# Kernel tuning notes

Hardware: AMD Instinct MI355X
Metric: run time of the kernel (lower is better)

## Reference

```python
import jax, jax.numpy as jnp
import numpy as np


def _greens(x, k0_raw, amp_raw):
    """Faithful TunableGreens: FFT-domain filtering with per-channel-pair Green's fn.
    NOTE: the source applies fftn over axes (0,1) (batch+H) but ifftn over axes (1,2)
    (H+W); we replicate that exactly."""
    H, W = x.shape[1], x.shape[2]
    k0 = jax.nn.softplus(k0_raw)    # (C, Co, 1, 1)
    amp = jax.nn.softplus(amp_raw)  # (C, Co, 1, 1)
    fy = (2.0 * jnp.pi) * jnp.fft.fftfreq(H, d=1.0).astype(jnp.float32)
    fx = (2.0 * jnp.pi) * jnp.fft.fftfreq(W, d=1.0).astype(jnp.float32)
    p = fy[:, None] ** 2 + fx[None, :] ** 2            # (H, W) = sum(freq_grid**2, -1)
    g_fourier = 1.0 / (amp * p - k0 - 1j)              # (C, Co, H, W) complex64
    u_fft = jnp.fft.fftn(x, axes=(0, 1))               # axes (0,1) as in source
    u_filtered = jnp.einsum('bijc,coij->bijo', u_fft, g_fourier)
    return jnp.fft.ifftn(u_filtered, axes=(1, 2)).real


def _D(Wm, x):
    # per-pixel channel mixing: x [b,i,j,c], Wm [b,i,j,c,o]
    return jnp.einsum('bijc,bijco->bijo', x, Wm)


def _project(k, W1, b1, W2, b2, W3, b3):
    act = lambda z: jnp.exp(-z ** 2)
    x = act(k @ W1 + b1)
    x = act(x @ W2 + b2)
    return x @ W3 + b3


def setup_inputs() -> dict:
    key = jax.random.key(0)
    ks = jax.random.split(key, 10)
    B, H, W, C = 2, 128, 128, 32
    d = {}
    d['u'] = jax.random.normal(ks[0], (B, H, W, C), jnp.float32)
    d['k'] = jax.random.normal(ks[1], (B, H, W, 1), jnp.float32)
    for i, n in enumerate(['g1', 'g2', 'g3', 'g4']):
        d[n] = jax.random.normal(ks[2 + i], (B, H, W, C, C), jnp.float32) * 0.1
    # Project MLP params (lecun-normal-ish scaling)
    d['W1'] = jax.random.normal(ks[6], (1, C), jnp.float32)
    d['b1'] = jnp.zeros((C,), jnp.float32)
    d['W2'] = jax.random.normal(ks[7], (C, C), jnp.float32) * (1.0 / np.sqrt(C))
    d['b2'] = jnp.zeros((C,), jnp.float32)
    d['W3'] = jax.random.normal(ks[8], (C, C), jnp.float32) * (1.0 / np.sqrt(C))
    d['b3'] = jnp.zeros((C,), jnp.float32)
    # TunableGreens params, constant(1.0) init as in source
    d['k0_G'] = jnp.ones((C, C, 1, 1), jnp.float32)
    d['amp_G'] = jnp.ones((C, C, 1, 1), jnp.float32)
    d['k0_Gs'] = jnp.ones((C, C, 1, 1), jnp.float32)
    d['amp_Gs'] = jnp.ones((C, C, 1, 1), jnp.float32)
    return d


def reference(u, k, g1, g2, g3, g4, W1, b1, W2, b2, W3, b3,
              k0_G, amp_G, k0_Gs, amp_Gs):
    s = _project(k, W1, b1, W2, b2, W3, b3)           # [B,H,W,C]
    u1 = _D(g4, _greens(s, k0_Gs, amp_Gs))
    u2 = _D(g1, _greens(_D(g2, u), k0_G, amp_G)) + _D(g3, u)
    return u1 + u2
```

## Files before the change

### kernel.cpp

```cpp
#include <hip/hip_runtime.h>

using u16 = unsigned short;
using u32 = unsigned int;

#define PI2 6.283185307179586f

struct cpx { float x, y; };

__device__ __forceinline__ float bf2f(u16 h){ return __uint_as_float(((u32)h) << 16); }
__device__ __forceinline__ u16 f2bf(float f){
  u32 u = __float_as_uint(f);
  u = u + 0x7fffu + ((u >> 16) & 1u);
  return (u16)(u >> 16);
}

__device__ __forceinline__ float ldv(const void* base, size_t i, int md){
  return md ? ((const float*)base)[i] : bf2f(((const u16*)base)[i]);
}

__device__ __forceinline__ cpx cadd(cpx a, cpx b){ return {a.x+b.x, a.y+b.y}; }
__device__ __forceinline__ cpx csub(cpx a, cpx b){ return {a.x-b.x, a.y-b.y}; }
__device__ __forceinline__ cpx cmul(cpx a, cpx b){ return {a.x*b.x - a.y*b.y, a.x*b.y + a.y*b.x}; }
__device__ __forceinline__ int br6(int l){ return (int)(__brev((u32)l) >> 26); }
__device__ __forceinline__ cpx shflx(cpx v, int m){
  cpx r; r.x = __shfl_xor(v.x, m, 64); r.y = __shfl_xor(v.y, m, 64); return r;
}

__device__ __forceinline__ void make_tw(int l, cpx tw[6]){
  #pragma unroll
  for (int s = 0; s < 6; s++){
    int h = 64 >> s;
    float ang = -PI2 * (float)(l & (h-1)) / (float)(2*h);
    float sv, cv; sincosf(ang, &sv, &cv);
    tw[s] = {cv, sv};
  }
}

__device__ __forceinline__ void fft_fwd(cpx& v0, cpx& v1, int l, const cpx tw[6]){
  cpx a = cadd(v0, v1), b = csub(v0, v1);
  v0 = a; v1 = cmul(b, tw[0]);
  #pragma unroll
  for (int s = 1; s < 6; s++){
    int h = 64 >> s;
    cpx p0 = shflx(v0, h), p1 = shflx(v1, h);
    bool up = (l & h) != 0;
    cpx n0 = up ? cmul(csub(p0, v0), tw[s]) : cadd(v0, p0);
    cpx n1 = up ? cmul(csub(p1, v1), tw[s]) : cadd(v1, p1);
    v0 = n0; v1 = n1;
  }
  { cpx p0 = shflx(v0, 1), p1 = shflx(v1, 1);
    bool up = (l & 1) != 0;
    v0 = up ? csub(p0, v0) : cadd(v0, p0);
    v1 = up ? csub(p1, v1) : cadd(v1, p1); }
}

__device__ __forceinline__ void fft_inv(cpx& v0, cpx& v1, int l, const cpx tw[6]){
  { cpx p0 = shflx(v0, 1), p1 = shflx(v1, 1);
    bool up = (l & 1) != 0;
    v0 = up ? csub(p0, v0) : cadd(v0, p0);
    v1 = up ? csub(p1, v1) : cadd(v1, p1); }
  #pragma unroll
  for (int s = 5; s >= 1; s--){
    int h = 64 >> s;
    cpx twc = {tw[s].x, -tw[s].y};
    cpx p0 = shflx(v0, h), p1 = shflx(v1, h);
    bool up = (l & h) != 0;
    cpx t0 = cmul(up ? v0 : p0, twc);
    cpx t1 = cmul(up ? v1 : p1, twc);
    v0 = up ? csub(p0, t0) : cadd(v0, t0);
    v1 = up ? csub(p1, t1) : cadd(v1, t1);
  }
  { cpx twc = {tw[0].x, -tw[0].y};
    cpx t = cmul(v1, twc);
    cpx n0 = cadd(v0, t), n1 = csub(v0, t);
    v0 = n0; v1 = n1; }
}

__device__ __forceinline__ float softplusf(float x){ return (x > 20.0f) ? x : log1pf(expf(x)); }

__device__ __forceinline__ void acc8_bf(uint4 a, uint4 b, float x0, float x1, float acc[8]){
  acc[0] = fmaf(x0, __uint_as_float(a.x << 16),         acc[0]);
  acc[1] = fmaf(x0, __uint_as_float(a.x & 0xffff0000u), acc[1]);
  acc[2] = fmaf(x0, __uint_as_float(a.y << 16),         acc[2]);
  acc[3] = fmaf(x0, __uint_as_float(a.y & 0xffff0000u), acc[3]);
  acc[4] = fmaf(x0, __uint_as_float(a.z << 16),         acc[4]);
  acc[5] = fmaf(x0, __uint_as_float(a.z & 0xffff0000u), acc[5]);
  acc[6] = fmaf(x0, __uint_as_float(a.w << 16),         acc[6]);
  acc[7] = fmaf(x0, __uint_as_float(a.w & 0xffff0000u), acc[7]);
  acc[0] = fmaf(x1, __uint_as_float(b.x << 16),         acc[0]);
  acc[1] = fmaf(x1, __uint_as_float(b.x & 0xffff0000u), acc[1]);
  acc[2] = fmaf(x1, __uint_as_float(b.y << 16),         acc[2]);
  acc[3] = fmaf(x1, __uint_as_float(b.y & 0xffff0000u), acc[3]);
  acc[4] = fmaf(x1, __uint_as_float(b.z << 16),         acc[4]);
  acc[5] = fmaf(x1, __uint_as_float(b.z & 0xffff0000u), acc[5]);
  acc[6] = fmaf(x1, __uint_as_float(b.w << 16),         acc[6]);
  acc[7] = fmaf(x1, __uint_as_float(b.w & 0xffff0000u), acc[7]);
}
__device__ __forceinline__ void acc8_f32(float4 a0, float4 a1, float4 b0, float4 b1,
                                         float x0, float x1, float acc[8]){
  acc[0] = fmaf(x0, a0.x, acc[0]); acc[1] = fmaf(x0, a0.y, acc[1]);
  acc[2] = fmaf(x0, a0.z, acc[2]); acc[3] = fmaf(x0, a0.w, acc[3]);
  acc[4] = fmaf(x0, a1.x, acc[4]); acc[5] = fmaf(x0, a1.y, acc[5]);
  acc[6] = fmaf(x0, a1.z, acc[6]); acc[7] = fmaf(x0, a1.w, acc[7]);
  acc[0] = fmaf(x1, b0.x, acc[0]); acc[1] = fmaf(x1, b0.y, acc[1]);
  acc[2] = fmaf(x1, b0.z, acc[2]); acc[3] = fmaf(x1, b0.w, acc[3]);
  acc[4] = fmaf(x1, b1.x, acc[4]); acc[5] = fmaf(x1, b1.y, acc[5]);
  acc[6] = fmaf(x1, b1.z, acc[6]); acc[7] = fmaf(x1, b1.w, acc[7]);
}

__global__ void k_detect(const void* g1, int* flag){
  __shared__ int cnt;
  if (threadIdx.x == 0) cnt = 0;
  __syncthreads();
  const u16* p = (const u16*)g1;
  int local = 0;
  for (int i = threadIdx.x; i < 4096; i += 256){
    float v = bf2f(p[i]);
    if (!(fabsf(v) < 100.0f)) local++;
  }
  atomicAdd(&cnt, local);
  __syncthreads();
  if (threadIdx.x == 0) *flag = (cnt > 64) ? 1 : 0;
}

__global__ void k_tabs(const void* k0G, const void* ampG, const void* k0Gs, const void* ampGs,
                       float* tabs, const int* flag){
  int md = *flag;
  for (int i = threadIdx.x; i < 1024; i += 256){
    tabs[i]        = softplusf(ldv(ampGs, i, md));
    tabs[1024 + i] = softplusf(ldv(k0Gs, i, md));
    tabs[2048 + i] = softplusf(ldv(ampG, i, md));
    tabs[3072 + i] = softplusf(ldv(k0G, i, md));
  }
}

__global__ __launch_bounds__(256) void k_project(const void* kin, const void* W1, const void* b1,
    const void* W2, const void* b2, const void* W3, const void* b3, float* S, const int* flag){
  __shared__ float sW2[1024], sW3[1024], sml[128];
  int md = *flag;
  int t = threadIdx.x;
  for (int i = t; i < 1024; i += 256){ sW2[i] = ldv(W2, i, md); sW3[i] = ldv(W3, i, md); }
  if (t < 32){
    sml[t]     = ldv(W1, t, md); sml[32+t] = ldv(b1, t, md);
    sml[64+t]  = ldv(b2, t, md); sml[96+t] = ldv(b3, t, md);
  }
  __syncthreads();
  int pix = blockIdx.x * 256 + t;
  float kv = ldv(kin, pix, md);
  float a1[32], a2[32];
  #pragma unroll
  for (int c = 0; c < 32; c++){ float z = fmaf(kv, sml[c], sml[32+c]); a1[c] = expf(-z*z); }
  for (int o = 0; o < 32; o++){
    float z = sml[64+o];
    #pragma unroll
    for (int c = 0; c < 32; c++) z = fmaf(a1[c], sW2[c*32+o], z);
    a2[o] = expf(-z*z);
  }
  for (int o = 0; o < 32; o++){
    float sv = sml[96+o];
    #pragma unroll
    for (int c = 0; c < 32; c++) sv = fmaf(a2[c], sW3[c*32+o], sv);
    S[(size_t)pix*32 + o] = sv;
  }
}

__global__ __launch_bounds__(256) void k_dmat(const void* u, const void* g2, float* D, const int* flag){
  int md = *flag;
  int t = threadIdx.x, l = t & 63;
  size_t pix = (size_t)blockIdx.x * 8 + (size_t)(t >> 6) * 2;
  int c32 = l & 31, ch = l >> 2;
  float xa = ldv(u, pix*32 + c32, md);
  float xb = ldv(u, (pix+1)*32 + c32, md);
  float acc0[8] = {0.f,0.f,0.f,0.f,0.f,0.f,0.f,0.f};
  float acc1[8] = {0.f,0.f,0.f,0.f,0.f,0.f,0.f,0.f};
  if (md){
    const float4* Ra = (const float4*)((const float*)g2 + pix*1024);
    const float4* Rb = (const float4*)((const float*)g2 + (pix+1)*1024);
    float4 aa = Ra[2*l], ab = Ra[2*l+1], ac = Ra[128+2*l], ad = Ra[128+2*l+1];
    float4 ba = Rb[2*l], bb = Rb[2*l+1], bc = Rb[128+2*l], bd = Rb[128+2*l+1];
    float xa0 = __shfl(xa, ch, 64), xa1 = __shfl(xa, 16+ch, 64);
    float xb0 = __shfl(xb, ch, 64), xb1 = __shfl(xb, 16+ch, 64);
    acc8_f32(aa, ab, ac, ad, xa0, xa1, acc0);
    acc8_f32(ba, bb, bc, bd, xb0, xb1, acc1);
  } else {
    const uint4* Ra = (const uint4*)((const u16*)g2 + pix*1024);
    const uint4* Rb = (const uint4*)((const u16*)g2 + (pix+1)*1024);
    uint4 a0 = Ra[l], a1 = Ra[64+l];
    uint4 b0 = Rb[l], b1 = Rb[64+l];
    float xa0 = __shfl(xa, ch, 64), xa1 = __shfl(xa, 16+ch, 64);
    float xb0 = __shfl(xb, ch, 64), xb1 = __shfl(xb, 16+ch, 64);
    acc8_bf(a0, a1, xa0, xa1, acc0);
    acc8_bf(b0, b1, xb0, xb1, acc1);
  }
  #pragma unroll
  for (int d = 4; d <= 32; d <<= 1){
    #pragma unroll
    for (int jj = 0; jj < 8; jj++){
      acc0[jj] += __shfl_xor(acc0[jj], d, 64);
      acc1[jj] += __shfl_xor(acc1[jj], d, 64);
    }
  }
  if (l < 4){
    ((float4*)(D + pix*32))[2*l]       = make_float4(acc0[0], acc0[1], acc0[2], acc0[3]);
    ((float4*)(D + pix*32))[2*l+1]     = make_float4(acc0[4], acc0[5], acc0[6], acc0[7]);
    ((float4*)(D + (pix+1)*32))[2*l]   = make_float4(acc1[0], acc1[1], acc1[2], acc1[3]);
    ((float4*)(D + (pix+1)*32))[2*l+1] = make_float4(acc1[4], acc1[5], acc1[6], acc1[7]);
  }
}

__global__ __launch_bounds__(512) void kg_a(const float* S, const float* Dd, const float* tabs, float2* Q){
  __shared__ __align__(16) cpx E[64*128];
  int t = threadIdx.x;
  int p = blockIdx.x >> 7, j = blockIdx.x & 127;
  const float* X = p ? Dd : S;
  const float* ampT = tabs + p*2048;
  const float* k0T  = ampT + 1024;
  int l = t & 63, w = t >> 6;
  cpx tw[6]; make_tw(l, tw);

  {
    int h = t >> 2, ch = (t & 3) * 8;
    const float4* x0 = (const float4*)(X + (((size_t)h)*128 + j)*32 + ch);
    const float4* x1 = (const float4*)(X + (((size_t)(128 + h))*128 + j)*32 + ch);
    #pragma unroll
    for (int q = 0; q < 2; q++){
      float4 A = x0[q], B = x1[q];
      int c = ch + q*4;
      E[(c+0)*128 + h] = {A.x+B.x, 0.f};  E[(32+c+0)*128 + h] = {A.x-B.x, 0.f};
      E[(c+1)*128 + h] = {A.y+B.y, 0.f};  E[(32+c+1)*128 + h] = {A.y-B.y, 0.f};
      E[(c+2)*128 + h] = {A.z+B.z, 0.f};  E[(32+c+2)*128 + h] = {A.z-B.z, 0.f};
      E[(c+3)*128 + h] = {A.w+B.w, 0.f};  E[(32+c+3)*128 + h] = {A.w-B.w, 0.f};
    }
  }
  __syncthreads();
  for (int c = w; c < 64; c += 8){
    cpx* col = E + c*128;
    cpx v0 = col[l], v1 = col[l+64];
    fft_fwd(v0, v1, l, tw);
    ((float4*)col)[br6(l)] = make_float4(v0.x, v0.y, v1.x, v1.y);
  }
  __syncthreads();
  {
    int o = t & 31, ig = t >> 5;
    float aT[32], kT[32];
    #pragma unroll
    for (int c = 0; c < 32; c++){ aT[c] = ampT[c*32+o]; kT[c] = k0T[c*32+o]; }
    float fj = (j < 64) ? (float)j : (float)(j - 128);
    fj *= (PI2 / 128.0f);
    float px = fj * fj;
    for (int chunk = 0; chunk < 2; chunk++){
      cpx y0[4], y1[4];
      #pragma unroll
      for (int q = 0; q < 4; q++){
        int i = ig + 16*(chunk*4 + q);
        float fi = (i < 64) ? (float)i : (float)(i - 128);
        fi *= (PI2 / 128.0f);
        float pp = fmaf(fi, fi, px);
        cpx a0 = {0.f, 0.f}, a1 = {0.f, 0.f};
        #pragma unroll
        for (int c = 0; c < 32; c++){
          float dd  = fmaf(aT[c], pp, -kT[c]);
          float inv = __builtin_amdgcn_rcpf(fmaf(dd, dd, 1.0f));
          float gr = dd * inv, gi = inv;
          cpx x0 = E[c*128 + i];
          cpx x1 = E[(32+c)*128 + i];
          a0.x = fmaf(x0.x, gr, fmaf(-x0.y, gi, a0.x));
          a0.y = fmaf(x0.x, gi, fmaf( x0.y, gr, a0.y));
          a1.x = fmaf(x1.x, gr, fmaf(-x1.y, gi, a1.x));
          a1.y = fmaf(x1.x, gi, fmaf( x1.y, gr, a1.y));
        }
        y0[q] = a0; y1[q] = a1;
      }
      __syncthreads();
      #pragma unroll
      for (int q = 0; q < 4; q++){
        int i = ig + 16*(chunk*4 + q);
        E[o*128 + i]      = y0[q];
        E[(32+o)*128 + i] = y1[q];
      }
      __syncthreads();
    }
  }
  for (int cidx = w; cidx < 64; cidx += 8){
    cpx* col = E + cidx*128;
    float4 tv = ((const float4*)col)[br6(l)];
    cpx v0 = {tv.x, tv.y}, v1 = {tv.z, tv.w};
    fft_inv(v0, v1, l, tw);
    const float sc = 1.0f/128.0f;
    col[l]    = {v0.x*sc, v0.y*sc};
    col[l+64] = {v1.x*sc, v1.y*sc};
  }
  __syncthreads();
  {
    int o = t & 31, bb = (t >> 5) & 1, yb = t >> 6;
    for (int m = 0; m < 16; m++){
      int y = yb + 8*m;
      cpx v = E[(bb*32+o)*128 + y];
      Q[((((size_t)(p*2+bb))*128 + y)*128 + j)*32 + o] = make_float2(v.x, v.y);
    }
  }
}

__global__ __launch_bounds__(256) void kg_c(const float2* Q, float* G0, float* G1){
  __shared__ __align__(16) cpx Z[32*128];
  __shared__ float R[32*128];
  int t = threadIdx.x, l = t & 63, w = t >> 6;
  int idx = blockIdx.x;
  int p = idx >> 8, rem = idx & 255, bb = rem >> 7, y = rem & 127;
  cpx tw[6]; make_tw(l, tw);
  const float4* src = (const float4*)(Q + ((size_t)((p*2+bb)*128 + y))*4096);
  for (int q = t; q < 2048; q += 256){
    float4 v = src[q];
    int m = q*2, jj = m >> 5, c = m & 31;
    Z[c*128 + jj]     = {v.x, v.y};
    Z[(c+1)*128 + jj] = {v.z, v.w};
  }
  __syncthreads();
  for (int c = w; c < 32; c += 4){
    cpx* col = Z + c*128;
    float4 tv = ((const float4*)col)[br6(l)];
    cpx v0 = {tv.x, tv.y}, v1 = {tv.z, tv.w};
    fft_inv(v0, v1, l, tw);
    R[c*128 + l]      = v0.x * (1.0f/128.0f);
    R[c*128 + l + 64] = v1.x * (1.0f/128.0f);
  }
  __syncthreads();
  float* dst = (p ? G1 : G0) + ((size_t)(bb*128 + y))*4096;
  int jj = t >> 3, c4 = (t & 7)*4;
  for (int rep = 0; rep < 4; rep++){
    int j2 = jj + rep*32;
    float4 o4 = { R[(c4+0)*128 + j2], R[(c4+1)*128 + j2],
                  R[(c4+2)*128 + j2], R[(c4+3)*128 + j2] };
    ((float4*)(dst + (size_t)j2*32))[c4 >> 2] = o4;
  }
}

__global__ __launch_bounds__(256) void k_final(const void* u, const void* g1, const void* g3, const void* g4,
    const float* G0, const float* G1, void* out, const int* flag){
  int md = *flag;
  int t = threadIdx.x, l = t & 63;
  size_t pix = (size_t)blockIdx.x * 4 + (t >> 6);
  int c32 = l & 31, ch = l >> 2;
  float xs = G0[pix*32 + c32];
  float xm = G1[pix*32 + c32];
  float xu = ldv(u, pix*32 + c32, md);
  float acc[8] = {0.f,0.f,0.f,0.f,0.f,0.f,0.f,0.f};
  if (md){
    const float4* R4 = (const float4*)((const float*)g4 + pix*1024);
    const float4* R1 = (const float4*)((const float*)g1 + pix*1024);
    const float4* R3 = (const float4*)((const float*)g3 + pix*1024);
    float4 p4a = R4[2*l], p4b = R4[2*l+1], q4a = R4[128+2*l], q4b = R4[128+2*l+1];
    float4 p1a = R1[2*l], p1b = R1[2*l+1], q1a = R1[128+2*l], q1b = R1[128+2*l+1];
    float4 p3a = R3[2*l], p3b = R3[2*l+1], q3a = R3[128+2*l], q3b = R3[128+2*l+1];
    float xs0 = __shfl(xs, ch, 64), xs1 = __shfl(xs, 16+ch, 64);
    float xm0 = __shfl(xm, ch, 64), xm1 = __shfl(xm, 16+ch, 64);
    float xu0 = __shfl(xu, ch, 64), xu1 = __shfl(xu, 16+ch, 64);
    acc8_f32(p4a, p4b, q4a, q4b, xs0, xs1, acc);
    acc8_f32(p1a, p1b, q1a, q1b, xm0, xm1, acc);
    acc8_f32(p3a, p3b, q3a, q3b, xu0, xu1, acc);
  } else {
    const uint4* R4 = (const uint4*)((const u16*)g4 + pix*1024);
    const uint4* R1 = (const uint4*)((const u16*)g1 + pix*1024);
    const uint4* R3 = (const uint4*)((const u16*)g3 + pix*1024);
    uint4 a4 = R4[l], b4 = R4[64+l];
    uint4 a1 = R1[l], b1 = R1[64+l];
    uint4 a3 = R3[l], b3 = R3[64+l];
    float xs0 = __shfl(xs, ch, 64), xs1 = __shfl(xs, 16+ch, 64);
    float xm0 = __shfl(xm, ch, 64), xm1 = __shfl(xm, 16+ch, 64);
    float xu0 = __shfl(xu, ch, 64), xu1 = __shfl(xu, 16+ch, 64);
    acc8_bf(a4, b4, xs0, xs1, acc);
    acc8_bf(a1, b1, xm0, xm1, acc);
    acc8_bf(a3, b3, xu0, xu1, acc);
  }
  #pragma unroll
  for (int d = 4; d <= 32; d <<= 1){
    #pragma unroll
    for (int jj = 0; jj < 8; jj++) acc[jj] += __shfl_xor(acc[jj], d, 64);
  }
  if (l < 4){
    if (md){
      float4 o0 = {acc[0], acc[1], acc[2], acc[3]};
      float4 o1 = {acc[4], acc[5], acc[6], acc[7]};
      ((float4*)out)[pix*8 + 2*l]     = o0;
      ((float4*)out)[pix*8 + 2*l + 1] = o1;
    } else {
      uint4 v;
      v.x = (u32)f2bf(acc[0]) | ((u32)f2bf(acc[1]) << 16);
      v.y = (u32)f2bf(acc[2]) | ((u32)f2bf(acc[3]) << 16);
      v.z = (u32)f2bf(acc[4]) | ((u32)f2bf(acc[5]) << 16);
      v.w = (u32)f2bf(acc[6]) | ((u32)f2bf(acc[7]) << 16);
      ((uint4*)out)[pix*4 + l] = v;
    }
  }
}

extern "C" void kernel_launch(void* const* d_in, const int* in_sizes, int n_in,
                              void* d_out, int out_size, void* d_ws, size_t ws_size,
                              hipStream_t stream){
  (void)in_sizes; (void)n_in; (void)out_size; (void)ws_size;
  const void* u    = d_in[0];
  const void* kk   = d_in[1];
  const void* g1   = d_in[2];
  const void* g2   = d_in[3];
  const void* g3   = d_in[4];
  const void* g4   = d_in[5];
  const void* W1   = d_in[6];
  const void* b1   = d_in[7];
  const void* W2   = d_in[8];
  const void* b2   = d_in[9];
  const void* W3   = d_in[10];
  const void* b3   = d_in[11];
  const void* k0G  = d_in[12];
  const void* ampG = d_in[13];
  const void* k0Gs = d_in[14];
  const void* ampGs= d_in[15];

  float* ws   = (float*)d_ws;
  float* S    = ws;
  float* Dd   = ws + (1u<<20);
  float2* Q   = (float2*)(ws + 2*(1u<<20));
  float* G0   = ws + 6*(1u<<20);
  float* G1b  = ws + 7*(1u<<20);
  float* tabs = ws + 8*(1u<<20);
  int*   flag = (int*)(tabs + 4096);

  k_detect <<<1,    256, 0, stream>>>(g1, flag);
  k_tabs   <<<1,    256, 0, stream>>>(k0G, ampG, k0Gs, ampGs, tabs, flag);
  k_project<<<128,  256, 0, stream>>>(kk, W1, b1, W2, b2, W3, b3, S, flag);
  k_dmat   <<<4096, 256, 0, stream>>>(u, g2, Dd, flag);
  kg_a     <<<256,  512, 0, stream>>>(S, Dd, tabs, Q);
  kg_c     <<<512,  256, 0, stream>>>(Q, G0, G1b);
  k_final  <<<8192, 256, 0, stream>>>(u, g1, g3, g4, G0, G1b, (void*)d_out, flag);
}
```

Baseline: 536.7 us.

## Use nontemporal loads for streamed weights, pad kg_c shared memory, split k_final

Loads of the streamed per-pixel matrices g2 and g3 now use nontemporal loads, so single-use data is less likely to evict useful cache lines. The kg_c shared arrays get padded row strides to cut LDS bank conflicts in the transpose and gather. k_final is split into two half-size launches with a pixel offset, which adds one launch of overhead for no clear gain.

New measurement: 538.9 us. About the same (+0.4%).

```diff
diff --git a/kernel.cpp b/kernel.cpp
--- a/kernel.cpp
+++ b/kernel.cpp
@@ -6,6 +6,18 @@
 #define PI2 6.283185307179586f
 
 struct cpx { float x, y; };
+
+typedef unsigned int uvec4 __attribute__((ext_vector_type(4)));
+typedef float fvec4 __attribute__((ext_vector_type(4)));
+
+__device__ __forceinline__ uint4 ldnt_u4(const uint4* p){
+  uvec4 v = __builtin_nontemporal_load((const uvec4*)p);
+  uint4 r; r.x = v.x; r.y = v.y; r.z = v.z; r.w = v.w; return r;
+}
+__device__ __forceinline__ float4 ldnt_f4(const float4* p){
+  fvec4 v = __builtin_nontemporal_load((const fvec4*)p);
+  float4 r; r.x = v.x; r.y = v.y; r.z = v.z; r.w = v.w; return r;
+}
 
 __device__ __forceinline__ float bf2f(u16 h){ return __uint_as_float(((u32)h) << 16); }
 __device__ __forceinline__ u16 f2bf(float f){
@@ -176,8 +188,8 @@
   if (md){
     const float4* Ra = (const float4*)((const float*)g2 + pix*1024);
     const float4* Rb = (const float4*)((const float*)g2 + (pix+1)*1024);
-    float4 aa = Ra[2*l], ab = Ra[2*l+1], ac = Ra[128+2*l], ad = Ra[128+2*l+1];
-    float4 ba = Rb[2*l], bb = Rb[2*l+1], bc = Rb[128+2*l], bd = Rb[128+2*l+1];
+    float4 aa = ldnt_f4(Ra+2*l), ab = ldnt_f4(Ra+2*l+1), ac = ldnt_f4(Ra+128+2*l), ad = ldnt_f4(Ra+128+2*l+1);
+    float4 ba = ldnt_f4(Rb+2*l), bb = ldnt_f4(Rb+2*l+1), bc = ldnt_f4(Rb+128+2*l), bd = ldnt_f4(Rb+128+2*l+1);
     float xa0 = __shfl(xa, ch, 64), xa1 = __shfl(xa, 16+ch, 64);
     float xb0 = __shfl(xb, ch, 64), xb1 = __shfl(xb, 16+ch, 64);
     acc8_f32(aa, ab, ac, ad, xa0, xa1, acc0);
@@ -185,8 +197,8 @@
   } else {
     const uint4* Ra = (const uint4*)((const u16*)g2 + pix*1024);
     const uint4* Rb = (const uint4*)((const u16*)g2 + (pix+1)*1024);
-    uint4 a0 = Ra[l], a1 = Ra[64+l];
-    uint4 b0 = Rb[l], b1 = Rb[64+l];
+    uint4 a0 = ldnt_u4(Ra+l), a1 = ldnt_u4(Ra+64+l);
+    uint4 b0 = ldnt_u4(Rb+l), b1 = ldnt_u4(Rb+64+l);
     float xa0 = __shfl(xa, ch, 64), xa1 = __shfl(xa, 16+ch, 64);
     float xb0 = __shfl(xb, ch, 64), xb1 = __shfl(xb, 16+ch, 64);
     acc8_bf(a0, a1, xa0, xa1, acc0);
@@ -301,9 +313,11 @@
   }
 }
 
+#define ZS 130
+#define RS 133
 __global__ __launch_bounds__(256) void kg_c(const float2* Q, float* G0, float* G1){
-  __shared__ __align__(16) cpx Z[32*128];
-  __shared__ float R[32*128];
+  __shared__ __align__(16) cpx Z[32*ZS];
+  __shared__ float R[32*RS];
   int t = threadIdx.x, l = t & 63, w = t >> 6;
   int idx = blockIdx.x;
   int p = idx >> 8, rem = idx & 255, bb = rem >> 7, y = rem & 127;
@@ -312,34 +326,34 @@
   for (int q = t; q < 2048; q += 256){
     float4 v = src[q];
     int m = q*2, jj = m >> 5, c = m & 31;
-    Z[c*128 + jj]     = {v.x, v.y};
-    Z[(c+1)*128 + jj] = {v.z, v.w};
+    Z[c*ZS + jj]     = {v.x, v.y};
+    Z[(c+1)*ZS + jj] = {v.z, v.w};
   }
   __syncthreads();
   for (int c = w; c < 32; c += 4){
-    cpx* col = Z + c*128;
+    cpx* col = Z + c*ZS;
     float4 tv = ((const float4*)col)[br6(l)];
     cpx v0 = {tv.x, tv.y}, v1 = {tv.z, tv.w};
     fft_inv(v0, v1, l, tw);
-    R[c*128 + l]      = v0.x * (1.0f/128.0f);
-    R[c*128 + l + 64] = v1.x * (1.0f/128.0f);
+    R[c*RS + l]      = v0.x * (1.0f/128.0f);
+    R[c*RS + l + 64] = v1.x * (1.0f/128.0f);
   }
   __syncthreads();
   float* dst = (p ? G1 : G0) + ((size_t)(bb*128 + y))*4096;
   int jj = t >> 3, c4 = (t & 7)*4;
   for (int rep = 0; rep < 4; rep++){
     int j2 = jj + rep*32;
-    float4 o4 = { R[(c4+0)*128 + j2], R[(c4+1)*128 + j2],
-                  R[(c4+2)*128 + j2], R[(c4+3)*128 + j2] };
+    float4 o4 = { R[(c4+0)*RS + j2], R[(c4+1)*RS + j2],
+                  R[(c4+2)*RS + j2], R[(c4+3)*RS + j2] };
     ((float4*)(dst + (size_t)j2*32))[c4 >> 2] = o4;
   }
 }
 
 __global__ __launch_bounds__(256) void k_final(const void* u, const void* g1, const void* g3, const void* g4,
-    const float* G0, const float* G1, void* out, const int* flag){
+    const float* G0, const float* G1, void* out, const int* flag, int pix0){
   int md = *flag;
   int t = threadIdx.x, l = t & 63;
-  size_t pix = (size_t)blockIdx.x * 4 + (t >> 6);
+  size_t pix = (size_t)pix0 + (size_t)blockIdx.x * 4 + (t >> 6);
   int c32 = l & 31, ch = l >> 2;
   float xs = G0[pix*32 + c32];
   float xm = G1[pix*32 + c32];
@@ -351,7 +365,7 @@
     const float4* R3 = (const float4*)((const float*)g3 + pix*1024);
     float4 p4a = R4[2*l], p4b = R4[2*l+1], q4a = R4[128+2*l], q4b = R4[128+2*l+1];
     float4 p1a = R1[2*l], p1b = R1[2*l+1], q1a = R1[128+2*l], q1b = R1[128+2*l+1];
-    float4 p3a = R3[2*l], p3b = R3[2*l+1], q3a = R3[128+2*l], q3b = R3[128+2*l+1];
+    float4 p3a = ldnt_f4(R3+2*l), p3b = ldnt_f4(R3+2*l+1), q3a = ldnt_f4(R3+128+2*l), q3b = ldnt_f4(R3+128+2*l+1);
     float xs0 = __shfl(xs, ch, 64), xs1 = __shfl(xs, 16+ch, 64);
     float xm0 = __shfl(xm, ch, 64), xm1 = __shfl(xm, 16+ch, 64);
     float xu0 = __shfl(xu, ch, 64), xu1 = __shfl(xu, 16+ch, 64);
@@ -364,7 +378,7 @@
     const uint4* R3 = (const uint4*)((const u16*)g3 + pix*1024);
     uint4 a4 = R4[l], b4 = R4[64+l];
     uint4 a1 = R1[l], b1 = R1[64+l];
-    uint4 a3 = R3[l], b3 = R3[64+l];
+    uint4 a3 = ldnt_u4(R3+l), b3 = ldnt_u4(R3+64+l);
     float xs0 = __shfl(xs, ch, 64), xs1 = __shfl(xs, 16+ch, 64);
     float xm0 = __shfl(xm, ch, 64), xm1 = __shfl(xm, 16+ch, 64);
     float xu0 = __shfl(xu, ch, 64), xu1 = __shfl(xu, 16+ch, 64);
@@ -430,5 +444,6 @@
   k_dmat   <<<4096, 256, 0, stream>>>(u, g2, Dd, flag);
   kg_a     <<<256,  512, 0, stream>>>(S, Dd, tabs, Q);
   kg_c     <<<512,  256, 0, stream>>>(Q, G0, G1b);
-  k_final  <<<8192, 256, 0, stream>>>(u, g1, g3, g4, G0, G1b, (void*)d_out, flag);
-}
+  k_final  <<<4096, 256, 0, stream>>>(u, g1, g3, g4, G0, G1b, (void*)d_out, flag, 0);
+  k_final  <<<4096, 256, 0, stream>>>(u, g1, g3, g4, G0, G1b, (void*)d_out, flag, 16384);
+}
```
